# Kernel tuning notes

Measured on AMD Instinct MI355X. Metric: run time of the kernel, lower is better.

The kernel has to match this reference:

```python
import jax, jax.numpy as jnp
import numpy as np

SIGMA = 1.0

def setup_inputs() -> dict:
    key = jax.random.key(0)
    k1, k2 = jax.random.split(key)
    N, IN, OUT = 524288, 64, 128
    x = jax.random.normal(k1, (N, IN), dtype=jnp.float32)
    bin_centers = jax.random.normal(k2, (OUT, IN), dtype=jnp.float32)
    return {"x": x, "bin_centers": bin_centers}

def reference(x, bin_centers):
    # distances[n,o] = sum_i (x[n,i] - c[o,i])^2 = ||x_n||^2 - 2 x_n.c_o + ||c_o||^2
    x2 = jnp.sum(x * x, axis=1)[:, None]                # [N,1]
    c2 = jnp.sum(bin_centers * bin_centers, axis=1)[None, :]  # [1,O]
    xc = jnp.einsum('ni,oi->no', x, bin_centers)        # [N,O] GEMM
    distances = x2 - 2.0 * xc + c2                      # [N,O]
    rbf = jnp.exp(-distances / (2.0 * SIGMA ** 2))      # [N,O]
    # histogram[o,i] = sum_n rbf[n,o] * x[n,i]  ->  rbf^T @ x
    histogram = jnp.einsum('no,ni->oi', rbf, x)         # [O,I] GEMM
    return histogram
```

## Files before the change

kernel.cpp:

```cpp
#include <hip/hip_runtime.h>
#include <stdint.h>


typedef __bf16 bf16x8 __attribute__((ext_vector_type(8)));
typedef unsigned short ushortx8 __attribute__((ext_vector_type(8)));
typedef float floatx4 __attribute__((ext_vector_type(4)));

#define GRIDN 1024
#define NITER 8
#define SCL 1.2011224087864498f

#if __has_builtin(__builtin_amdgcn_exp2f)
#define EXP2F(x) __builtin_amdgcn_exp2f(x)
#else
#define EXP2F(x) exp2f(x)
#endif

static __device__ __forceinline__ unsigned int bfbits(float f) {
  unsigned int u = __float_as_uint(f);
  return u + 0x7fffu + ((u >> 16) & 1u);
}
static __device__ __forceinline__ unsigned int pkbf(float a, float b) {
  return (bfbits(a) >> 16) | (bfbits(b) & 0xffff0000u);
}

static __device__ __forceinline__ floatx4 mfma_bf16(ushortx8 a, ushortx8 b, floatx4 c) {
  return __builtin_amdgcn_mfma_f32_16x16x32_bf16(
      __builtin_bit_cast(bf16x8, a), __builtin_bit_cast(bf16x8, b), c, 0, 0, 0);
}

#define LSTR 72
#define PSTR 40

__global__ __launch_bounds__(256, 4) void rbf_hist_kernel(
    const float* __restrict__ x, const float* __restrict__ c,
    float* __restrict__ out, float* __restrict__ ws, int use_ws) {
  __shared__ unsigned short sXhi[64][LSTR];
  __shared__ unsigned short sXlo[64][LSTR];
  __shared__ unsigned short sXT [64][LSTR];
  __shared__ unsigned short sPw [4][32][PSTR];
  __shared__ float          sX2 [64];

  const int t    = threadIdx.x;
  const int lane = t & 63;
  const int w    = t >> 6;
  const int l15  = lane & 15;
  const int quad = lane >> 4;

  uint4 chi[2][2], clo[2][2];
  float m2c[2];
#pragma unroll
  for (int oo = 0; oo < 2; ++oo) {
    const int ot = 2 * w + oo;
    float sq = 0.f;
#pragma unroll
    for (int s = 0; s < 2; ++s) {
      const float* p = c + (ot * 16 + l15) * 64 + s * 32 + quad * 8;
      float4 va = *(const float4*)(p);
      float4 vb = *(const float4*)(p + 4);
      float f[8] = {va.x, va.y, va.z, va.w, vb.x, vb.y, vb.z, vb.w};
      unsigned int h[4], l[4];
#pragma unroll
      for (int jp = 0; jp < 4; ++jp) {
        float a = f[2 * jp] * SCL, b = f[2 * jp + 1] * SCL;
        sq = fmaf(a, a, sq);
        sq = fmaf(b, b, sq);
        unsigned int hp = pkbf(a, b);
        float la = a - __uint_as_float(hp << 16);
        float lb = b - __uint_as_float(hp & 0xffff0000u);
        h[jp] = hp;
        l[jp] = pkbf(la, lb);
      }
      chi[oo][s] = uint4{h[0], h[1], h[2], h[3]};
      clo[oo][s] = uint4{l[0], l[1], l[2], l[3]};
    }
    sq += __shfl_xor(sq, 16);
    sq += __shfl_xor(sq, 32);
    m2c[oo] = -0.5f * sq;
  }

  floatx4 hacc[2][4];
#pragma unroll
  for (int a = 0; a < 2; ++a)
#pragma unroll
    for (int b = 0; b < 4; ++b) {
      floatx4 z = {0.f, 0.f, 0.f, 0.f};
      hacc[a][b] = z;
    }

  const int r = t >> 2, q = t & 3;
  float4 v[4];
  {
    const size_t row0 = (size_t)(blockIdx.x * 64 + r) * 64;
#pragma unroll
    for (int g = 0; g < 4; ++g)
      v[g] = *(const float4*)(x + row0 + q * 4 + g * 16);
  }

  for (int it = 0; it < NITER; ++it) {
    __syncthreads();

    {
      float sq = 0.f;
#pragma unroll
      for (int g = 0; g < 4; ++g) {
        const int col = q * 4 + g * 16;
        float f0 = v[g].x, f1 = v[g].y, f2 = v[g].z, f3 = v[g].w;
        unsigned int u01 = pkbf(f0, f1), u23 = pkbf(f2, f3);
        sXT[col + 0][r] = (unsigned short)(u01 & 0xffffu);
        sXT[col + 1][r] = (unsigned short)(u01 >> 16);
        sXT[col + 2][r] = (unsigned short)(u23 & 0xffffu);
        sXT[col + 3][r] = (unsigned short)(u23 >> 16);
        float s0 = f0 * SCL, s1 = f1 * SCL, s2 = f2 * SCL, s3 = f3 * SCL;
        sq = fmaf(s0, s0, sq); sq = fmaf(s1, s1, sq);
        sq = fmaf(s2, s2, sq); sq = fmaf(s3, s3, sq);
        unsigned int h01 = pkbf(s0, s1), h23 = pkbf(s2, s3);
        float l0 = s0 - __uint_as_float(h01 << 16);
        float l1 = s1 - __uint_as_float(h01 & 0xffff0000u);
        float l2 = s2 - __uint_as_float(h23 << 16);
        float l3 = s3 - __uint_as_float(h23 & 0xffff0000u);
        uint2 hh = {h01, h23};
        uint2 ll = {pkbf(l0, l1), pkbf(l2, l3)};
        *(uint2*)&sXhi[r][col] = hh;
        *(uint2*)&sXlo[r][col] = ll;
      }
      sq += __shfl_xor(sq, 1);
      sq += __shfl_xor(sq, 2);
      if (q == 0) sX2[r] = -0.5f * sq;
    }
    __syncthreads();

    if (it < NITER - 1) {
      const size_t nrow = (size_t)((blockIdx.x + (it + 1) * GRIDN) * 64 + r) * 64;
#pragma unroll
      for (int g = 0; g < 4; ++g)
        v[g] = *(const float4*)(x + nrow + q * 4 + g * 16);
    }

#pragma unroll
    for (int p = 0; p < 2; ++p) {
#pragma unroll
      for (int u = 0; u < 2; ++u) {
        const int nt = 2 * p + u;
        ushortx8 xh0 = *(const ushortx8*)&sXhi[nt * 16 + l15][quad * 8];
        ushortx8 xh1 = *(const ushortx8*)&sXhi[nt * 16 + l15][32 + quad * 8];
        ushortx8 xl0 = *(const ushortx8*)&sXlo[nt * 16 + l15][quad * 8];
        ushortx8 xl1 = *(const ushortx8*)&sXlo[nt * 16 + l15][32 + quad * 8];
        float4 m2x = *(const float4*)&sX2[nt * 16 + quad * 4];

#pragma unroll
        for (int oo = 0; oo < 2; ++oo) {
          floatx4 accA = {m2x.x + m2c[oo], m2x.y + m2c[oo],
                          m2x.z + m2c[oo], m2x.w + m2c[oo]};
          floatx4 accB = {0.f, 0.f, 0.f, 0.f};
          accA = mfma_bf16(xh0, __builtin_bit_cast(ushortx8, chi[oo][0]), accA);
          accB = mfma_bf16(xh1, __builtin_bit_cast(ushortx8, clo[oo][1]), accB);
          accA = mfma_bf16(xh1, __builtin_bit_cast(ushortx8, chi[oo][1]), accA);
          accB = mfma_bf16(xl0, __builtin_bit_cast(ushortx8, chi[oo][0]), accB);
          accA = mfma_bf16(xh0, __builtin_bit_cast(ushortx8, clo[oo][0]), accA);
          accB = mfma_bf16(xl1, __builtin_bit_cast(ushortx8, chi[oo][1]), accB);
          floatx4 acc = accA + accB;
          unsigned int r01 = pkbf(EXP2F(acc[0]), EXP2F(acc[1]));
          unsigned int r23 = pkbf(EXP2F(acc[2]), EXP2F(acc[3]));
          unsigned short* bp = &sPw[w][oo * 16 + l15][u * 16 + quad * 4];
          *(unsigned int*)(bp)     = r01;
          *(unsigned int*)(bp + 2) = r23;
        }
      }
      ushortx8 a0 = *(const ushortx8*)&sPw[w][l15][quad * 8];
      ushortx8 a1 = *(const ushortx8*)&sPw[w][16 + l15][quad * 8];
#pragma unroll
      for (int itl = 0; itl < 4; ++itl) {
        ushortx8 b = *(const ushortx8*)&sXT[itl * 16 + l15][p * 32 + quad * 8];
        hacc[0][itl] = mfma_bf16(a0, b, hacc[0][itl]);
        hacc[1][itl] = mfma_bf16(a1, b, hacc[1][itl]);
      }
    }
  }

  if (use_ws) {
    float* part = ws + (size_t)blockIdx.x * 8192;
#pragma unroll
    for (int oi = 0; oi < 2; ++oi)
#pragma unroll
      for (int itl = 0; itl < 4; ++itl)
#pragma unroll
        for (int e = 0; e < 4; ++e) {
          int o = (2 * w + oi) * 16 + quad * 4 + e;
          int i = itl * 16 + l15;
          part[o * 64 + i] = hacc[oi][itl][e];
        }
  } else {
#pragma unroll
    for (int oi = 0; oi < 2; ++oi)
#pragma unroll
      for (int itl = 0; itl < 4; ++itl)
#pragma unroll
        for (int e = 0; e < 4; ++e) {
          int o = (2 * w + oi) * 16 + quad * 4 + e;
          int i = itl * 16 + l15;
          atomicAdd(out + o * 64 + i, hacc[oi][itl][e]);
        }
  }
}

__global__ void reduce_kernel(const float* __restrict__ ws, float* __restrict__ out) {
  const int tid = blockIdx.x * 256 + threadIdx.x;
  const int e = tid & 8191;
  const int part = tid >> 13;
  const float* p = ws + (size_t)part * 256 * 8192 + e;
  float s = 0.f;
#pragma unroll 8
  for (int b = 0; b < 256; ++b) s += p[(size_t)b * 8192];
  atomicAdd(out + e, s);
}

__global__ void zero_out_kernel(float* out, int n) {
  int i = blockIdx.x * 256 + threadIdx.x;
  if (i < n) out[i] = 0.f;
}

extern "C" void kernel_launch(void* const* d_in, const int* in_sizes, int n_in,
                              void* d_out, int out_size, void* d_ws, size_t ws_size,
                              hipStream_t stream) {
  (void)in_sizes; (void)n_in;
  const float* x = (const float*)d_in[0];
  const float* c = (const float*)d_in[1];
  float* out = (float*)d_out;
  float* ws  = (float*)d_ws;

  const int use_ws = (ws_size >= (size_t)GRIDN * 8192 * sizeof(float)) ? 1 : 0;

  zero_out_kernel<<<(out_size + 255) / 256, 256, 0, stream>>>(out, out_size);
  rbf_hist_kernel<<<GRIDN, 256, 0, stream>>>(x, c, out, ws, use_ws);
  if (use_ws)
    reduce_kernel<<<128, 256, 0, stream>>>(ws, out);
}
```

Measured before the change: 212.4 us.

## Use two-wave blocks covering all outputs and fold log2e into centers only

The main kernel drops from four waves per block to two. Each wave now computes four output tiles over a 32-row strip, instead of two tiles over a 64-row strip, which raises per-wave register reuse of the x fragments. The log2(e) scaling now applies only to the centers and the squared-norm terms, so the x high bf16 split can be reused directly for the transposed operand, saving a conversion. The trade-off is fewer resident waves in total (launch bounds 128,2) and twice as many barrier-separated strip iterations, which may hurt latency hiding.

```diff
diff --git a/kernel.cpp b/kernel.cpp
--- a/kernel.cpp
+++ b/kernel.cpp
@@ -7,8 +7,8 @@
 typedef float floatx4 __attribute__((ext_vector_type(4)));
 
 #define GRIDN 1024
-#define NITER 8
-#define SCL 1.2011224087864498f
+#define NSTRIPS 16384
+#define LOG2E 1.4426950408889634f
 
 #if __has_builtin(__builtin_amdgcn_exp2f)
 #define EXP2F(x) __builtin_amdgcn_exp2f(x)
@@ -32,14 +32,14 @@
 #define LSTR 72
 #define PSTR 40
 
-__global__ __launch_bounds__(256, 4) void rbf_hist_kernel(
+__global__ __launch_bounds__(128, 2) void rbf_hist_kernel(
     const float* __restrict__ x, const float* __restrict__ c,
     float* __restrict__ out, float* __restrict__ ws, int use_ws) {
-  __shared__ unsigned short sXhi[64][LSTR];
-  __shared__ unsigned short sXlo[64][LSTR];
-  __shared__ unsigned short sXT [64][LSTR];
-  __shared__ unsigned short sPw [4][32][PSTR];
-  __shared__ float          sX2 [64];
+  __shared__ unsigned short sXhi[32][LSTR];
+  __shared__ unsigned short sXlo[32][LSTR];
+  __shared__ unsigned short sXT [64][PSTR];
+  __shared__ unsigned short sPw [2][64][PSTR];
+  __shared__ float          sX2 [32];
 
   const int t    = threadIdx.x;
   const int lane = t & 63;
@@ -47,11 +47,11 @@
   const int l15  = lane & 15;
   const int quad = lane >> 4;
 
-  uint4 chi[2][2], clo[2][2];
-  float m2c[2];
-#pragma unroll
-  for (int oo = 0; oo < 2; ++oo) {
-    const int ot = 2 * w + oo;
+  uint4 chi[4][2], clo[4][2];
+  float m2c[4];
+#pragma unroll
+  for (int oo = 0; oo < 4; ++oo) {
+    const int ot = 4 * w + oo;
     float sq = 0.f;
 #pragma unroll
     for (int s = 0; s < 2; ++s) {
@@ -62,9 +62,10 @@
       unsigned int h[4], l[4];
 #pragma unroll
       for (int jp = 0; jp < 4; ++jp) {
-        float a = f[2 * jp] * SCL, b = f[2 * jp + 1] * SCL;
+        float a = f[2 * jp], b = f[2 * jp + 1];
         sq = fmaf(a, a, sq);
         sq = fmaf(b, b, sq);
+        a *= LOG2E; b *= LOG2E;
         unsigned int hp = pkbf(a, b);
         float la = a - __uint_as_float(hp << 16);
         float lb = b - __uint_as_float(hp & 0xffff0000u);
@@ -76,12 +77,12 @@
     }
     sq += __shfl_xor(sq, 16);
     sq += __shfl_xor(sq, 32);
-    m2c[oo] = -0.5f * sq;
-  }
-
-  floatx4 hacc[2][4];
-#pragma unroll
-  for (int a = 0; a < 2; ++a)
+    m2c[oo] = -0.5f * LOG2E * sq;
+  }
+
+  floatx4 hacc[4][4];
+#pragma unroll
+  for (int a = 0; a < 4; ++a)
 #pragma unroll
     for (int b = 0; b < 4; ++b) {
       floatx4 z = {0.f, 0.f, 0.f, 0.f};
@@ -91,13 +92,13 @@
   const int r = t >> 2, q = t & 3;
   float4 v[4];
   {
-    const size_t row0 = (size_t)(blockIdx.x * 64 + r) * 64;
+    const size_t row0 = (size_t)(blockIdx.x * 32 + r) * 64;
 #pragma unroll
     for (int g = 0; g < 4; ++g)
       v[g] = *(const float4*)(x + row0 + q * 4 + g * 16);
   }
 
-  for (int it = 0; it < NITER; ++it) {
+  for (int it = 0; it < NSTRIPS / GRIDN; ++it) {
     __syncthreads();
 
     {
@@ -106,74 +107,75 @@
       for (int g = 0; g < 4; ++g) {
         const int col = q * 4 + g * 16;
         float f0 = v[g].x, f1 = v[g].y, f2 = v[g].z, f3 = v[g].w;
-        unsigned int u01 = pkbf(f0, f1), u23 = pkbf(f2, f3);
-        sXT[col + 0][r] = (unsigned short)(u01 & 0xffffu);
-        sXT[col + 1][r] = (unsigned short)(u01 >> 16);
-        sXT[col + 2][r] = (unsigned short)(u23 & 0xffffu);
-        sXT[col + 3][r] = (unsigned short)(u23 >> 16);
-        float s0 = f0 * SCL, s1 = f1 * SCL, s2 = f2 * SCL, s3 = f3 * SCL;
-        sq = fmaf(s0, s0, sq); sq = fmaf(s1, s1, sq);
-        sq = fmaf(s2, s2, sq); sq = fmaf(s3, s3, sq);
-        unsigned int h01 = pkbf(s0, s1), h23 = pkbf(s2, s3);
-        float l0 = s0 - __uint_as_float(h01 << 16);
-        float l1 = s1 - __uint_as_float(h01 & 0xffff0000u);
-        float l2 = s2 - __uint_as_float(h23 << 16);
-        float l3 = s3 - __uint_as_float(h23 & 0xffff0000u);
+        sq = fmaf(f0, f0, sq); sq = fmaf(f1, f1, sq);
+        sq = fmaf(f2, f2, sq); sq = fmaf(f3, f3, sq);
+        unsigned int h01 = pkbf(f0, f1), h23 = pkbf(f2, f3);
+        float l0 = f0 - __uint_as_float(h01 << 16);
+        float l1 = f1 - __uint_as_float(h01 & 0xffff0000u);
+        float l2 = f2 - __uint_as_float(h23 << 16);
+        float l3 = f3 - __uint_as_float(h23 & 0xffff0000u);
         uint2 hh = {h01, h23};
         uint2 ll = {pkbf(l0, l1), pkbf(l2, l3)};
         *(uint2*)&sXhi[r][col] = hh;
         *(uint2*)&sXlo[r][col] = ll;
+        sXT[col + 0][r] = (unsigned short)(h01 & 0xffffu);
+        sXT[col + 1][r] = (unsigned short)(h01 >> 16);
+        sXT[col + 2][r] = (unsigned short)(h23 & 0xffffu);
+        sXT[col + 3][r] = (unsigned short)(h23 >> 16);
       }
       sq += __shfl_xor(sq, 1);
       sq += __shfl_xor(sq, 2);
-      if (q == 0) sX2[r] = -0.5f * sq;
+      if (q == 0) sX2[r] = -0.5f * LOG2E * sq;
     }
     __syncthreads();
 
-    if (it < NITER - 1) {
-      const size_t nrow = (size_t)((blockIdx.x + (it + 1) * GRIDN) * 64 + r) * 64;
+    if (it < NSTRIPS / GRIDN - 1) {
+      const size_t nrow = (size_t)((blockIdx.x + (it + 1) * GRIDN) * 32 + r) * 64;
 #pragma unroll
       for (int g = 0; g < 4; ++g)
         v[g] = *(const float4*)(x + nrow + q * 4 + g * 16);
     }
 
 #pragma unroll
-    for (int p = 0; p < 2; ++p) {
-#pragma unroll
-      for (int u = 0; u < 2; ++u) {
-        const int nt = 2 * p + u;
-        ushortx8 xh0 = *(const ushortx8*)&sXhi[nt * 16 + l15][quad * 8];
-        ushortx8 xh1 = *(const ushortx8*)&sXhi[nt * 16 + l15][32 + quad * 8];
-        ushortx8 xl0 = *(const ushortx8*)&sXlo[nt * 16 + l15][quad * 8];
-        ushortx8 xl1 = *(const ushortx8*)&sXlo[nt * 16 + l15][32 + quad * 8];
-        float4 m2x = *(const float4*)&sX2[nt * 16 + quad * 4];
-
-#pragma unroll
-        for (int oo = 0; oo < 2; ++oo) {
-          floatx4 accA = {m2x.x + m2c[oo], m2x.y + m2c[oo],
-                          m2x.z + m2c[oo], m2x.w + m2c[oo]};
-          floatx4 accB = {0.f, 0.f, 0.f, 0.f};
-          accA = mfma_bf16(xh0, __builtin_bit_cast(ushortx8, chi[oo][0]), accA);
-          accB = mfma_bf16(xh1, __builtin_bit_cast(ushortx8, clo[oo][1]), accB);
-          accA = mfma_bf16(xh1, __builtin_bit_cast(ushortx8, chi[oo][1]), accA);
-          accB = mfma_bf16(xl0, __builtin_bit_cast(ushortx8, chi[oo][0]), accB);
-          accA = mfma_bf16(xh0, __builtin_bit_cast(ushortx8, clo[oo][0]), accA);
-          accB = mfma_bf16(xl1, __builtin_bit_cast(ushortx8, chi[oo][1]), accB);
-          floatx4 acc = accA + accB;
-          unsigned int r01 = pkbf(EXP2F(acc[0]), EXP2F(acc[1]));
-          unsigned int r23 = pkbf(EXP2F(acc[2]), EXP2F(acc[3]));
-          unsigned short* bp = &sPw[w][oo * 16 + l15][u * 16 + quad * 4];
-          *(unsigned int*)(bp)     = r01;
-          *(unsigned int*)(bp + 2) = r23;
-        }
-      }
-      ushortx8 a0 = *(const ushortx8*)&sPw[w][l15][quad * 8];
-      ushortx8 a1 = *(const ushortx8*)&sPw[w][16 + l15][quad * 8];
+    for (int t2 = 0; t2 < 2; ++t2) {
+      ushortx8 xh0 = *(const ushortx8*)&sXhi[t2 * 16 + l15][quad * 8];
+      ushortx8 xh1 = *(const ushortx8*)&sXhi[t2 * 16 + l15][32 + quad * 8];
+      ushortx8 xl0 = *(const ushortx8*)&sXlo[t2 * 16 + l15][quad * 8];
+      ushortx8 xl1 = *(const ushortx8*)&sXlo[t2 * 16 + l15][32 + quad * 8];
+      float4 m2x = *(const float4*)&sX2[t2 * 16 + quad * 4];
+
+#pragma unroll
+      for (int oo = 0; oo < 4; ++oo) {
+        floatx4 accA = {m2x.x + m2c[oo], m2x.y + m2c[oo],
+                        m2x.z + m2c[oo], m2x.w + m2c[oo]};
+        floatx4 accB = {0.f, 0.f, 0.f, 0.f};
+        accA = mfma_bf16(xh0, __builtin_bit_cast(ushortx8, chi[oo][0]), accA);
+        accB = mfma_bf16(xh1, __builtin_bit_cast(ushortx8, clo[oo][1]), accB);
+        accA = mfma_bf16(xh1, __builtin_bit_cast(ushortx8, chi[oo][1]), accA);
+        accB = mfma_bf16(xl0, __builtin_bit_cast(ushortx8, chi[oo][0]), accB);
+        accA = mfma_bf16(xh0, __builtin_bit_cast(ushortx8, clo[oo][0]), accA);
+        accB = mfma_bf16(xl1, __builtin_bit_cast(ushortx8, chi[oo][1]), accB);
+        floatx4 acc = accA + accB;
+        unsigned int r01 = pkbf(EXP2F(acc[0]), EXP2F(acc[1]));
+        unsigned int r23 = pkbf(EXP2F(acc[2]), EXP2F(acc[3]));
+        unsigned short* bp = &sPw[w][oo * 16 + l15][t2 * 16 + quad * 4];
+        *(unsigned int*)(bp)     = r01;
+        *(unsigned int*)(bp + 2) = r23;
+      }
+    }
+
+    {
+      ushortx8 a0 = *(const ushortx8*)&sPw[w][0 * 16 + l15][quad * 8];
+      ushortx8 a1 = *(const ushortx8*)&sPw[w][1 * 16 + l15][quad * 8];
+      ushortx8 a2 = *(const ushortx8*)&sPw[w][2 * 16 + l15][quad * 8];
+      ushortx8 a3 = *(const ushortx8*)&sPw[w][3 * 16 + l15][quad * 8];
 #pragma unroll
       for (int itl = 0; itl < 4; ++itl) {
-        ushortx8 b = *(const ushortx8*)&sXT[itl * 16 + l15][p * 32 + quad * 8];
+        ushortx8 b = *(const ushortx8*)&sXT[itl * 16 + l15][quad * 8];
         hacc[0][itl] = mfma_bf16(a0, b, hacc[0][itl]);
         hacc[1][itl] = mfma_bf16(a1, b, hacc[1][itl]);
+        hacc[2][itl] = mfma_bf16(a2, b, hacc[2][itl]);
+        hacc[3][itl] = mfma_bf16(a3, b, hacc[3][itl]);
       }
     }
   }
@@ -181,25 +183,25 @@
   if (use_ws) {
     float* part = ws + (size_t)blockIdx.x * 8192;
 #pragma unroll
-    for (int oi = 0; oi < 2; ++oi)
+    for (int oo = 0; oo < 4; ++oo)
 #pragma unroll
       for (int itl = 0; itl < 4; ++itl)
 #pragma unroll
         for (int e = 0; e < 4; ++e) {
-          int o = (2 * w + oi) * 16 + quad * 4 + e;
+          int o = (4 * w + oo) * 16 + quad * 4 + e;
           int i = itl * 16 + l15;
-          part[o * 64 + i] = hacc[oi][itl][e];
+          part[o * 64 + i] = hacc[oo][itl][e];
         }
   } else {
 #pragma unroll
-    for (int oi = 0; oi < 2; ++oi)
+    for (int oo = 0; oo < 4; ++oo)
 #pragma unroll
       for (int itl = 0; itl < 4; ++itl)
 #pragma unroll
         for (int e = 0; e < 4; ++e) {
-          int o = (2 * w + oi) * 16 + quad * 4 + e;
+          int o = (4 * w + oo) * 16 + quad * 4 + e;
           int i = itl * 16 + l15;
-          atomicAdd(out + o * 64 + i, hacc[oi][itl][e]);
+          atomicAdd(out + o * 64 + i, hacc[oo][itl][e]);
         }
   }
 }
@@ -232,7 +234,7 @@
   const int use_ws = (ws_size >= (size_t)GRIDN * 8192 * sizeof(float)) ? 1 : 0;
 
   zero_out_kernel<<<(out_size + 255) / 256, 256, 0, stream>>>(out, out_size);
-  rbf_hist_kernel<<<GRIDN, 256, 0, stream>>>(x, c, out, ws, use_ws);
+  rbf_hist_kernel<<<GRIDN, 128, 0, stream>>>(x, c, out, ws, use_ws);
   if (use_ws)
     reduce_kernel<<<128, 256, 0, stream>>>(ws, out);
 }
```

New measurement: 214.4 us. Within noise of the previous version (+0.9%).
